# Kernel optimization log

Hardware: AMD Instinct MI355X
Metric: run time of the kernel (lower is better)

The kernel has to match this reference:

```python
import jax, jax.numpy as jnp
import numpy as np

B, T, R, A = 4, 40, 2000, 36864
H = W = 64
C = 256
PP = 7
RED = 16.0
NCLS = 21
NPOS = 64   # rois_per_image*B//4
NNEG = 192  # rois_per_image*B*3//4
DH = 1024

def _iou(b1, b2):
    # boxes are (top,left,bottom,right)
    t = jnp.maximum(b1[..., 0], b2[..., 0])
    l = jnp.maximum(b1[..., 1], b2[..., 1])
    b = jnp.minimum(b1[..., 2], b2[..., 2])
    r = jnp.minimum(b1[..., 3], b2[..., 3])
    inter = jnp.clip(b - t, 0.0) * jnp.clip(r - l, 0.0)
    a1 = (b1[..., 2] - b1[..., 0]) * (b1[..., 3] - b1[..., 1])
    a2 = (b2[..., 2] - b2[..., 0]) * (b2[..., 3] - b2[..., 1])
    return inter / (a1 + a2 - inter)

def _smooth_l1(p, t):
    d = jnp.abs(p - t)
    return jnp.mean(jnp.where(d < 1.0, 0.5 * d * d, d - 0.5))

def _roi_pool(fm, rois):
    # fm [B,C,H,W], rois [N,5] = (img_id, top,left,bottom,right) in feature-map coords
    fmt = jnp.transpose(fm, (0, 2, 3, 1))  # [B,H,W,C]
    n = rois[:, 0].astype(jnp.int32)[:, None, None]
    t, l, b, r = rois[:, 1], rois[:, 2], rois[:, 3], rois[:, 4]
    g = (jnp.arange(PP, dtype=fm.dtype) + 0.5) / PP
    ys = jnp.clip(t[:, None] + g * (b - t)[:, None], 0.0, H - 1.0)
    xs = jnp.clip(l[:, None] + g * (r - l)[:, None], 0.0, W - 1.0)
    y0 = jnp.floor(ys).astype(jnp.int32)
    x0 = jnp.floor(xs).astype(jnp.int32)
    y1 = jnp.minimum(y0 + 1, H - 1)
    x1 = jnp.minimum(x0 + 1, W - 1)
    wy = (ys - y0)[:, :, None, None]
    wx = (xs - x0)[:, None, :, None]
    def gat(yi, xi):
        return fmt[n, yi[:, :, None], xi[:, None, :], :]  # [N,PP,PP,C]
    v = (gat(y0, x0) * (1 - wy) * (1 - wx) + gat(y0, x1) * (1 - wy) * wx
         + gat(y1, x0) * wy * (1 - wx) + gat(y1, x1) * wy * wx)
    return v.reshape(v.shape[0], -1)  # [N, PP*PP*C]

def _forward(nms_reg, nms_cls, feature_maps, bboxes, classes, anchors, rpn_reg, rpn_cls, W1, b1, Wr, br, Wc, bc):
    # ---------------- RPN trainer: anchor/target matching ----------------
    iou_a = _iou(bboxes[:, :, None, :], anchors[None, None, :, :])   # [B,T,A]
    max_iou = jnp.max(iou_a, axis=1)                                  # [B,A]
    tidx = jnp.argmax(iou_a, axis=1)
    max_tgt = jnp.take_along_axis(bboxes, jnp.broadcast_to(tidx[:, :, None], (B, A, 4)), axis=1)
    mask = (max_iou > 0.5).reshape(-1)
    pos = jnp.nonzero(mask, size=128)[0]        # first 128 positives, flat order (matches cls[mask][:128])
    neg = jnp.nonzero(~mask, size=256 - B)[0]   # torch quirk: 256 - len(mask_matched) = 256 - B
    clsf = rpn_cls.reshape(-1)
    logits = jnp.concatenate([clsf[pos], clsf[neg]])
    lbl = jnp.concatenate([jnp.ones(128, dtype=logits.dtype), jnp.zeros(256 - B, dtype=logits.dtype)])
    rpn_cls_loss = jnp.mean(jnp.maximum(logits, 0) - logits * lbl + jnp.log1p(jnp.exp(-jnp.abs(logits))))
    anc_f = jnp.broadcast_to(anchors[None], (B, A, 4)).reshape(-1, 4)
    rpn_reg_loss = _smooth_l1(rpn_reg.reshape(-1, 4)[pos], max_tgt.reshape(-1, 4)[pos] - anc_f[pos]) / 4.0

    # ------------- RCNN trainer: proposal matching + sampling -------------
    iou_r = _iou(nms_reg[:, None, :, :], bboxes[:, :, None, :])  # [B,T,R]
    iou_m = jnp.max(iou_r, axis=1)                               # [B,R]
    ridx = jnp.argmax(iou_r, axis=1)
    iou_f = iou_m.reshape(-1)
    posr = jnp.nonzero(iou_f > 0.5, size=NPOS)[0]                # first NPOS positives, flat order
    negscore = jnp.where(iou_f <= 0.5, iou_f, -jnp.inf)
    negr = jax.lax.top_k(negscore, NNEG)[1]                      # negatives sorted by IoU descending
    cls_g = jnp.take_along_axis(classes, ridx, axis=1).reshape(-1)
    cls_s = jnp.concatenate([cls_g[posr], jnp.zeros(NNEG, dtype=cls_g.dtype)])
    imid = jnp.repeat(jnp.arange(B, dtype=nms_reg.dtype), R)
    nmsf = nms_reg.reshape(-1, 4)
    sel = jnp.concatenate([posr, negr])
    rois = jnp.concatenate([imid[sel][:, None], nmsf[sel]], axis=1)  # [256,5]
    feat = _roi_pool(feature_maps, rois)
    hmid = jax.nn.relu(feat @ W1 + b1)
    rreg = hmid @ Wr + br
    rcls = hmid @ Wc + bc
    logp = jax.nn.log_softmax(rcls, axis=-1)
    rcnn_cls_loss = -jnp.mean(jnp.take_along_axis(logp, cls_s[:, None], axis=1))
    posb = nmsf[posr]
    rounded = jnp.concatenate([jnp.floor(posb[:, :2] * RED), jnp.ceil(posb[:, 2:] * RED)], axis=1) / RED
    mb = jnp.take_along_axis(bboxes, jnp.broadcast_to(ridx[:, :, None], (B, R, 4)), axis=1).reshape(-1, 4)[posr]
    tgt = mb - rounded
    pr = rreg[:NPOS]
    rcnn_reg_loss = sum(_smooth_l1(pr[:, c], tgt[:, c]) for c in range(4)) / 4.0
    offset = sum(jnp.mean(jnp.abs(pr[:, c] - tgt[:, c])) for c in range(4)) / 4.0
    acc = jnp.mean((jnp.argmax(rcls[:NPOS], axis=-1) == cls_s[:NPOS]).astype(jnp.float32))
    return rpn_cls_loss, rpn_reg_loss, rcnn_cls_loss, rcnn_reg_loss, acc, offset

def _boxes(k, shape):
    k1, k2 = jax.random.split(k)
    c = jax.random.uniform(k1, shape + (2,), minval=10.0, maxval=54.0)
    h = jax.random.uniform(k2, shape + (2,), minval=3.0, maxval=8.0)
    return jnp.concatenate([c - h, c + h], axis=-1)  # (top,left,bottom,right)

def setup_inputs():
    key = jax.random.key(0)
    ks = jax.random.split(key, 13)
    base = _boxes(ks[0], (T,))
    shift = jax.random.uniform(ks[1], (B, T, 2), minval=-0.2, maxval=0.2)
    bboxes = base[None] + jnp.concatenate([shift, shift], axis=-1)  # guarantees >=128 RPN positives
    classes = jax.random.randint(ks[2], (B, T), 1, NCLS)
    anchors = _boxes(ks[3], (A,)).at[:T].set(base)
    nms_reg = _boxes(ks[4], (B, R))
    shift2 = jax.random.uniform(ks[5], (B, T, 2), minval=-0.1, maxval=0.1)
    nms_reg = nms_reg.at[:, :T].set(bboxes + jnp.concatenate([shift2, shift2], axis=-1))  # >=64 RCNN positives
    nms_cls = jax.random.normal(ks[6], (B, R))
    feature_maps = jax.random.normal(ks[7], (B, C, H, W))
    rpn_reg = 0.1 * jax.random.normal(ks[8], (B, A, 4))
    rpn_cls = jax.random.normal(ks[9], (B, A))
    D = PP * PP * C
    W1 = jax.random.normal(ks[10], (D, DH)) * float(1.0 / np.sqrt(D))
    b1 = jnp.zeros((DH,))
    Wr = jax.random.normal(ks[11], (DH, 4)) * float(1.0 / np.sqrt(DH))
    br = jnp.zeros((4,))
    Wc = jax.random.normal(ks[12], (DH, NCLS)) * float(1.0 / np.sqrt(DH))
    bc = jnp.zeros((NCLS,))
    return dict(nms_reg=nms_reg, nms_cls=nms_cls, feature_maps=feature_maps, bboxes=bboxes,
                classes=classes, anchors=anchors, rpn_reg=rpn_reg, rpn_cls=rpn_cls,
                W1=W1, b1=b1, Wr=Wr, br=br, Wc=Wc, bc=bc)

def reference(nms_reg, nms_cls, feature_maps, bboxes, classes, anchors, rpn_reg, rpn_cls, W1, b1, Wr, br, Wc, bc):
    return _forward(nms_reg, nms_cls, feature_maps, bboxes, classes, anchors, rpn_reg, rpn_cls, W1, b1, Wr, br, Wc, bc)
```

## Files before the change

### kernel.cpp

```cpp
#include <hip/hip_runtime.h>

typedef unsigned short u16;
typedef unsigned long long u64;

constexpr int cB = 4, cT = 40, cR = 2000, cA = 36864;
constexpr int cH = 64, cW = 64, cC = 256, cPP = 7;
constexpr int cNCLS = 21, cNPOS = 64, cNNEG = 192, cDH = 1024;
constexpr int cD = cPP * cPP * cC;
constexpr int cBA = cB * cA;
constexpr int cBR = cB * cR;
constexpr int NW64 = cBA / 64;
constexpr int SPLITS = 14;
constexpr int KCH = cD / SPLITS;
constexpr int BK = 64;
constexpr int NITER = KCH / BK;
constexpr unsigned POSKEY = 0x007FFFFFu;

constexpr size_t O_TIDX  = 0;
constexpr size_t O_MASKW = 589824;
constexpr size_t O_KEYS  = 608256;
constexpr size_t O_RIDXG = 640256;
constexpr size_t O_SEL   = 672256;
constexpr size_t O_CLS   = 673280;
constexpr size_t O_ROIS  = 674304;
constexpr size_t O_TGT   = 678400;
constexpr size_t O_FMT   = 1048576;
constexpr size_t O_FEAT  = O_FMT + 8388608;
constexpr size_t O_CPART = O_FEAT + 6422528;

__device__ __forceinline__ float b2f(u16 u) {
  return __uint_as_float(((unsigned)u) << 16);
}
__device__ __forceinline__ u16 f2b(float f) {
  unsigned x = __float_as_uint(f);
  unsigned r = x + 0x7FFFu + ((x >> 16) & 1u);
  return (u16)(r >> 16);
}
__device__ __forceinline__ unsigned f2key(float f) {
  unsigned b = __float_as_uint(f);
  return b ^ ((b & 0x80000000u) ? 0xFFFFFFFFu : 0x80000000u);
}

typedef __attribute__((ext_vector_type(8))) short short8;
typedef __attribute__((ext_vector_type(4))) float f32x4;

__global__ __launch_bounds__(256) void k_front(
    const float* __restrict__ bboxes, const float* __restrict__ anchors,
    const float* __restrict__ nms_reg, const float* __restrict__ fm,
    int* __restrict__ tidx, u64* __restrict__ maskw,
    unsigned* __restrict__ keys, int* __restrict__ ridxg,
    u16* __restrict__ fmt) {
  __shared__ float sfm[64 * 65];
  int bid = blockIdx.x;
  if (bid < 576) {
    float* sb = sfm;
    int b = bid / 144;
    if (threadIdx.x < cT * 4) sb[threadIdx.x] = bboxes[b * cT * 4 + threadIdx.x];
    __syncthreads();
    int i = bid * 256 + threadIdx.x;
    int a = i - b * cA;
    float4 av = ((const float4*)anchors)[a];
    float at = av.x, al = av.y, ab = av.z, ar = av.w;
    float area_a = (ab - at) * (ar - al);
    float best = -1.0f; int bi = 0;
    for (int t = 0; t < cT; ++t) {
      float bt = sb[t * 4], bl = sb[t * 4 + 1], bbv = sb[t * 4 + 2], brv = sb[t * 4 + 3];
      float ih = fmaxf(fminf(bbv, ab) - fmaxf(bt, at), 0.0f);
      float iw = fmaxf(fminf(brv, ar) - fmaxf(bl, al), 0.0f);
      float inter = ih * iw;
      float a1 = (bbv - bt) * (brv - bl);
      float iou = inter / (a1 + area_a - inter);
      if (iou > best) { best = iou; bi = t; }
    }
    tidx[i] = bi;
    u64 bal = __ballot(best > 0.5f);
    if ((threadIdx.x & 63) == 0) maskw[i >> 6] = bal;
  } else if (bid < 608) {
    float* sb = sfm;
    for (int j = threadIdx.x; j < cB * cT * 4; j += 256) sb[j] = bboxes[j];
    __syncthreads();
    int i = (bid - 576) * 256 + threadIdx.x;
    if (i >= cBR) return;
    int b = i / cR;
    float4 nv = ((const float4*)nms_reg)[i];
    float nt = nv.x, nl = nv.y, nb = nv.z, nr = nv.w;
    float area_n = (nb - nt) * (nr - nl);
    float best = -1.0f; int bi = 0;
    for (int t = 0; t < cT; ++t) {
      const float* bx = &sb[(b * cT + t) * 4];
      float ih = fmaxf(fminf(bx[2], nb) - fmaxf(bx[0], nt), 0.0f);
      float iw = fmaxf(fminf(bx[3], nr) - fmaxf(bx[1], nl), 0.0f);
      float inter = ih * iw;
      float a1 = (bx[2] - bx[0]) * (bx[3] - bx[1]);
      float iou = inter / (a1 + area_n - inter);
      if (iou > best) { best = iou; bi = t; }
    }
    keys[i] = (best <= 0.5f) ? f2key(best) : POSKEY;
    ridxg[i] = bi;
  } else {
    int f = bid - 608;
    int b = f >> 8;
    int c0 = ((f >> 6) & 3) * 64;
    int p0 = (f & 63) * 64;
    int t = threadIdx.x;
    int pL = (t & 15) * 4, cL = t >> 4;
    #pragma unroll
    for (int i = 0; i < 4; ++i) {
      int c = cL + i * 16;
      float4 v = *(const float4*)&fm[((size_t)b * cC + c0 + c) * (cH * cW) + p0 + pL];
      sfm[c * 65 + pL] = v.x; sfm[c * 65 + pL + 1] = v.y;
      sfm[c * 65 + pL + 2] = v.z; sfm[c * 65 + pL + 3] = v.w;
    }
    __syncthreads();
    int pW = t >> 2, cg = (t & 3) * 16;
    unsigned pk[8];
    #pragma unroll
    for (int j = 0; j < 8; ++j) {
      unsigned lo = f2b(sfm[(cg + 2 * j) * 65 + pW]);
      unsigned hi = f2b(sfm[(cg + 2 * j + 1) * 65 + pW]);
      pk[j] = lo | (hi << 16);
    }
    u16* dst = &fmt[((size_t)b * (cH * cW) + p0 + pW) * cC + c0 + cg];
    *(uint4*)dst = *(uint4*)&pk[0];
    *(uint4*)(dst + 8) = *(uint4*)&pk[4];
  }
}

__global__ __launch_bounds__(1024) void k_select(
    const u64* __restrict__ maskw, const int* __restrict__ tidx,
    const float* __restrict__ rpn_cls, const float* __restrict__ rpn_reg,
    const float* __restrict__ bboxes, const float* __restrict__ anchors,
    const unsigned* __restrict__ keysg, const int* __restrict__ ridxg,
    const float* __restrict__ nms_reg, const int* __restrict__ classes,
    int* __restrict__ sel, int* __restrict__ cls_s,
    float* __restrict__ rois, float* __restrict__ tgt,
    float* __restrict__ out) {
  __shared__ __align__(16) char smem[50688];
  __shared__ float s_scalF[2];
  __shared__ int s_scalI[3];
  int tid = threadIdx.x, lane = tid & 63, w = tid >> 6;
  u64 lmask = (1ULL << lane) - 1ULL;

  if (blockIdx.x == 0) {
    if (tid < 4) out[2 + tid] = 0.0f;
    u64* s_w   = (u64*)smem;
    int* s_pre = (int*)(smem + 18432);
    int* s_cw  = (int*)(smem + 19008);
    int* s_pos = (int*)(smem + 19584);
    int* s_neg = (int*)(smem + 20096);
    for (int k = tid; k < NW64; k += 1024) s_w[k] = maskw[k];
    if (tid < 128) s_pos[tid] = 0;
    if (tid < 252) s_neg[tid] = 0;
    if (tid == 0) { s_scalF[0] = 0.0f; s_scalF[1] = 0.0f; }
    __syncthreads();
    if (tid < 144) {
      int c = 0;
      #pragma unroll
      for (int k2 = 0; k2 < 16; ++k2) c += __popcll(s_w[tid * 16 + k2]);
      s_cw[tid] = c;
    }
    __syncthreads();
    if (tid == 0) {
      int run = 0;
      for (int ch = 0; ch < 144; ++ch) { s_pre[ch] = run; run += s_cw[ch]; }
    }
    __syncthreads();
    for (int ch = w; ch < 144; ch += 16) {
      int pbase = s_pre[ch];
      int nbase = ch * 1024 - pbase;
      if (pbase >= 128 && nbase >= 252) continue;
      int pc = 0;
      #pragma unroll
      for (int s2 = 0; s2 < 16; ++s2) {
        u64 word = s_w[ch * 16 + s2];
        bool m = (word >> lane) & 1ULL;
        int prefP = __popcll(word & lmask);
        int idx = ch * 1024 + s2 * 64 + lane;
        if (m) {
          int g = pbase + pc + prefP;
          if (g < 128) s_pos[g] = idx;
        } else {
          int g = nbase + (s2 * 64 + lane) - (pc + prefP);
          if (g < 252) s_neg[g] = idx;
        }
        pc += __popcll(word);
      }
    }
    __syncthreads();
    if (tid < 380) {
      int flat; float lbl;
      if (tid < 128) { flat = s_pos[tid]; lbl = 1.0f; }
      else           { flat = s_neg[tid - 128]; lbl = 0.0f; }
      float l = rpn_cls[flat];
      float term = fmaxf(l, 0.0f) - l * lbl + log1pf(expf(-fabsf(l)));
      atomicAdd(&s_scalF[0], term);
    }
    if (tid < 512) {
      int j = tid >> 2, c = tid & 3;
      int flat = s_pos[j];
      int b = flat / cA, a = flat - b * cA;
      int t = tidx[flat];
      float p = rpn_reg[flat * 4 + c];
      float tg = bboxes[(b * cT + t) * 4 + c] - anchors[a * 4 + c];
      float d = fabsf(p - tg);
      float sl = (d < 1.0f) ? 0.5f * d * d : d - 0.5f;
      atomicAdd(&s_scalF[1], sl);
    }
    __syncthreads();
    if (tid == 0) {
      out[0] = s_scalF[0] / 380.0f;
      out[1] = s_scalF[1] / 512.0f / 4.0f;
    }
  } else {
    unsigned* s_key = (unsigned*)smem;
    int* s_hist = (int*)(smem + 32000);
    int* s_pc   = (int*)(smem + 48384);
    int* s_wsum = (int*)(smem + 48896);
    int* s_wsuf = (int*)(smem + 48960);
    int* s_posr = (int*)(smem + 49024);
    int* s_negr = (int*)(smem + 49280);

    for (int i = tid; i < cBR; i += 1024) s_key[i] = keysg[i];
    if (tid < 64) s_posr[tid] = 0;
    __syncthreads();

    {
      int myv = 0; int mypre[8];
      #pragma unroll
      for (int p = 0; p < 8; ++p) {
        int i = p * 1024 + tid;
        bool v = (i < cBR) && (s_key[i] == POSKEY);
        u64 bal = __ballot(v);
        if (lane == 0) s_pc[p * 16 + w] = __popcll(bal);
        mypre[p] = __popcll(bal & lmask);
        myv |= v ? (1 << p) : 0;
      }
      __syncthreads();
      if (tid == 0) {
        int run = 0;
        for (int k = 0; k < 128; ++k) { int t = s_pc[k]; s_pc[k] = run; run += t; }
      }
      __syncthreads();
      #pragma unroll
      for (int p = 0; p < 8; ++p) {
        if (myv & (1 << p)) {
          int g = s_pc[p * 16 + w] + mypre[p];
          if (g < 64) s_posr[g] = p * 1024 + tid;
        }
      }
    }

    unsigned thr = 0; int G = 0;
    int need = cNNEG;
    #pragma unroll
    for (int lvl = 0; lvl < 3; ++lvl) {
      __syncthreads();
      #pragma unroll
      for (int k = 0; k < 4; ++k) s_hist[tid * 4 + k] = 0;
      __syncthreads();
      #pragma unroll
      for (int p = 0; p < 8; ++p) {
        int i = p * 1024 + tid;
        if (i < cBR) {
          unsigned key = s_key[i];
          int bkt = -1;
          if (lvl == 0) bkt = key >> 20;
          else if (lvl == 1) { if ((key >> 20) == (thr >> 20)) bkt = (key >> 8) & 0xFFF; }
          else { if ((key >> 8) == (thr >> 8)) bkt = (key & 0xFF) << 4; }
          if (bkt >= 0) atomicAdd(&s_hist[bkt], 1);
        }
      }
      __syncthreads();
      int local0 = s_hist[tid * 4 + 0], local1 = s_hist[tid * 4 + 1];
      int local2 = s_hist[tid * 4 + 2], local3 = s_hist[tid * 4 + 3];
      int lsum = local0 + local1 + local2 + local3;
      int x = lsum;
      #pragma unroll
      for (int off = 1; off < 64; off <<= 1) {
        int t = __shfl_down(x, off, 64);
        if (lane + off < 64) x += t;
      }
      if (lane == 0) s_wsum[w] = x;
      __syncthreads();
      if (tid == 0) {
        int run = 0;
        for (int wi = 15; wi >= 0; --wi) { s_wsuf[wi] = run; run += s_wsum[wi]; }
      }
      __syncthreads();
      int above = s_wsuf[w] + (x - lsum);
      int run = above;
      int loc[4] = {local3, local2, local1, local0};
      #pragma unroll
      for (int j = 0; j < 4; ++j) {
        int S = run + loc[j];
        if (run < need && S >= need) { s_scalI[0] = tid * 4 + (3 - j); s_scalI[1] = run; }
        run = S;
      }
      __syncthreads();
      int bS = s_scalI[0], ov = s_scalI[1];
      if (lvl == 0) thr = ((unsigned)bS) << 20;
      else if (lvl == 1) thr |= ((unsigned)bS) << 8;
      else thr |= ((unsigned)bS) >> 4;
      G += ov;
      need -= ov;
    }

    if (tid == 0) s_scalI[2] = 0;
    __syncthreads();
    #pragma unroll
    for (int p = 0; p < 8; ++p) {
      int i = p * 1024 + tid;
      if (i < cBR && s_key[i] > thr) {
        int slot = atomicAdd(&s_scalI[2], 1);
        s_negr[slot] = i;
      }
    }
    {
      __syncthreads();
      int myv = 0; int mypre[8];
      #pragma unroll
      for (int p = 0; p < 8; ++p) {
        int i = p * 1024 + tid;
        bool v = (i < cBR) && (s_key[i] == thr);
        u64 bal = __ballot(v);
        if (lane == 0) s_pc[p * 16 + w] = __popcll(bal);
        mypre[p] = __popcll(bal & lmask);
        myv |= v ? (1 << p) : 0;
      }
      __syncthreads();
      if (tid == 0) {
        int run = 0;
        for (int k = 0; k < 128; ++k) { int t = s_pc[k]; s_pc[k] = run; run += t; }
      }
      __syncthreads();
      #pragma unroll
      for (int p = 0; p < 8; ++p) {
        if (myv & (1 << p)) {
          int g = s_pc[p * 16 + w] + mypre[p];
          if (g < need) s_negr[G + g] = p * 1024 + tid;
        }
      }
    }
    __syncthreads();

    if (tid < 256) {
      int flat = (tid < 64) ? s_posr[tid] : s_negr[tid - 64];
      sel[tid] = flat;
      int b = flat / cR;
      #pragma unroll
      for (int c = 0; c < 4; ++c) rois[tid * 4 + c] = nms_reg[flat * 4 + c];
      cls_s[tid] = (tid < 64) ? classes[b * cT + ridxg[flat]] : 0;
      if (tid < 64) {
        int mt = ridxg[flat];
        #pragma unroll
        for (int c = 0; c < 4; ++c) {
          float v = nms_reg[flat * 4 + c];
          float rr = ((c < 2) ? floorf(v * 16.0f) : ceilf(v * 16.0f)) / 16.0f;
          float mbv = bboxes[(b * cT + mt) * 4 + c];
          tgt[tid * 4 + c] = mbv - rr;
        }
      }
    }
  }
}

__global__ void k_roi_pool(const u16* __restrict__ fmt, const float* __restrict__ rois,
                           const int* __restrict__ sel, u16* __restrict__ feat) {
  int j = blockIdx.x;
  int py = blockIdx.y;
  int c = threadIdx.x;
  int flat = sel[j];
  int n = flat / cR;
  float t = rois[j * 4 + 0], l = rois[j * 4 + 1];
  float bb = rois[j * 4 + 2], r = rois[j * 4 + 3];
  const u16* base = fmt + (size_t)n * (cH * cW) * cC;
  float gy = (py + 0.5f) / (float)cPP;
  float ys = fminf(fmaxf(t + gy * (bb - t), 0.0f), 63.0f);
  int y0 = (int)floorf(ys);
  int y1 = min(y0 + 1, 63);
  float wy = ys - (float)y0;
  #pragma unroll
  for (int px = 0; px < cPP; ++px) {
    float gx = (px + 0.5f) / (float)cPP;
    float xs = fminf(fmaxf(l + gx * (r - l), 0.0f), 63.0f);
    int x0 = (int)floorf(xs);
    int x1 = min(x0 + 1, 63);
    float wx = xs - (float)x0;
    float f00 = b2f(base[(y0 * cW + x0) * cC + c]);
    float f01 = b2f(base[(y0 * cW + x1) * cC + c]);
    float f10 = b2f(base[(y1 * cW + x0) * cC + c]);
    float f11 = b2f(base[(y1 * cW + x1) * cC + c]);
    float v = f00 * (1.0f - wy) * (1.0f - wx) + f01 * (1.0f - wy) * wx +
              f10 * wy * (1.0f - wx) + f11 * wy * wx;
    feat[((size_t)j * 49 + py * cPP + px) * cC + c] = f2b(v);
  }
}

__global__ __launch_bounds__(256) void k_gemm1(const u16* __restrict__ feat, const float* __restrict__ W1,
                                               float* __restrict__ Cpart) {
  __shared__ u16 Bs[2][32][64];
  int tid = threadIdx.x;
  int bid = blockIdx.x;
  int ksp = bid >> 5;
  int n0 = (bid & 31) * 32;
  int kb0 = ksp * KCH;
  int lane = tid & 63, w = tid >> 6;
  int r = lane & 15, q = lane >> 4;
  int rb = r & 7;

  f32x4 acc[4][2] = {};

  int bn = tid & 31, kq = tid >> 5;
  int bswz = (kq ^ (bn & 7)) * 8;
  const float* bp = &W1[(size_t)(kb0 + kq * 8) * cDH + n0 + bn];

  int offK0 = (q ^ rb) * 8;
  int offK1 = ((4 + q) ^ rb) * 8;

  const u16* afp = &feat[(size_t)(w * 64 + r) * cD + kb0 + q * 8];

  float fE[8], fO[8];
  short8 aE[4][2], aO[4][2];

#define LOADB(f) { \
    _Pragma("unroll") \
    for (int j = 0; j < 8; ++j) f[j] = bp[(size_t)j * cDH]; \
    bp += (size_t)BK * cDH; }
#define STOREB(buf, f) { \
    union { u16 u[8]; uint4 v; } pb; \
    _Pragma("unroll") \
    for (int j = 0; j < 8; ++j) pb.u[j] = f2b(f[j]); \
    *(uint4*)&Bs[buf][bn][bswz] = pb.v; }
#define LOADA(dst, itv) { \
    const u16* _p = afp + (itv) * 64; \
    _Pragma("unroll") \
    for (int mf = 0; mf < 4; ++mf) { \
      dst[mf][0] = *(const short8*)(_p + (size_t)mf * 16 * cD); \
      dst[mf][1] = *(const short8*)(_p + (size_t)mf * 16 * cD + 32); \
    } }
#define COMPUTE(buf, a) { \
    short8 b00 = *(const short8*)&Bs[buf][r][offK0]; \
    short8 b10 = *(const short8*)&Bs[buf][16 + r][offK0]; \
    short8 b01 = *(const short8*)&Bs[buf][r][offK1]; \
    short8 b11 = *(const short8*)&Bs[buf][16 + r][offK1]; \
    _Pragma("unroll") \
    for (int mf = 0; mf < 4; ++mf) { \
      acc[mf][0] = __builtin_amdgcn_mfma_f32_16x16x32_bf16(a[mf][0], b00, acc[mf][0], 0, 0, 0); \
      acc[mf][1] = __builtin_amdgcn_mfma_f32_16x16x32_bf16(a[mf][0], b10, acc[mf][1], 0, 0, 0); \
      acc[mf][0] = __builtin_amdgcn_mfma_f32_16x16x32_bf16(a[mf][1], b01, acc[mf][0], 0, 0, 0); \
      acc[mf][1] = __builtin_amdgcn_mfma_f32_16x16x32_bf16(a[mf][1], b11, acc[mf][1], 0, 0, 0); \
    } }

  LOADB(fE);
  LOADB(fO);
  STOREB(0, fE);
  LOADA(aE, 0);
  LOADB(fE);
  __syncthreads();

  for (int it = 0; it < NITER; it += 2) {
    STOREB(1, fO);
    if (it + 3 < NITER) LOADB(fO);
    LOADA(aO, it + 1);
    COMPUTE(0, aE);
    __syncthreads();
    if (it + 2 < NITER) {
      STOREB(0, fE);
      if (it + 4 < NITER) LOADB(fE);
      LOADA(aE, it + 2);
    }
    COMPUTE(1, aO);
    __syncthreads();
  }

#undef LOADB
#undef STOREB
#undef LOADA
#undef COMPUTE

  float* Cp = Cpart + (size_t)ksp * 256 * cDH;
  #pragma unroll
  for (int mf = 0; mf < 4; ++mf) {
    #pragma unroll
    for (int rg = 0; rg < 4; ++rg) {
      int row = w * 64 + mf * 16 + q * 4 + rg;
      Cp[(size_t)row * cDH + n0 + r] = acc[mf][0][rg];
      Cp[(size_t)row * cDH + n0 + 16 + r] = acc[mf][1][rg];
    }
  }
}

__global__ __launch_bounds__(256) void k_heads(
    const float* __restrict__ Cpart, const float* __restrict__ b1,
    const float* __restrict__ Wr, const float* __restrict__ br,
    const float* __restrict__ Wc, const float* __restrict__ bc,
    const int* __restrict__ cls_s, const float* __restrict__ tgt,
    float* __restrict__ out) {
  __shared__ float sacc[25];
  int row = blockIdx.x, tid = threadIdx.x, lane = tid & 63;
  if (tid < 25) sacc[tid] = 0.0f;
  __syncthreads();
  int k0 = tid * 4;
  float4 h = *(const float4*)&b1[k0];
  #pragma unroll
  for (int s = 0; s < SPLITS; ++s) {
    float4 c = *(const float4*)&Cpart[(size_t)s * 256 * cDH + (size_t)row * cDH + k0];
    h.x += c.x; h.y += c.y; h.z += c.z; h.w += c.w;
  }
  float hv[4] = {fmaxf(h.x, 0.f), fmaxf(h.y, 0.f), fmaxf(h.z, 0.f), fmaxf(h.w, 0.f)};
  float part[25];
  #pragma unroll
  for (int c = 0; c < 25; ++c) part[c] = 0.0f;
  #pragma unroll
  for (int j = 0; j < 4; ++j) {
    float4 wr = *(const float4*)&Wr[(k0 + j) * 4];
    part[0] += hv[j] * wr.x; part[1] += hv[j] * wr.y;
    part[2] += hv[j] * wr.z; part[3] += hv[j] * wr.w;
    const float* wc = &Wc[(k0 + j) * 21];
    #pragma unroll
    for (int c = 0; c < 21; ++c) part[4 + c] += hv[j] * wc[c];
  }
  #pragma unroll
  for (int off = 32; off; off >>= 1) {
    #pragma unroll
    for (int c = 0; c < 25; ++c) part[c] += __shfl_down(part[c], off, 64);
  }
  if (lane == 0) {
    #pragma unroll
    for (int c = 0; c < 25; ++c) atomicAdd(&sacc[c], part[c]);
  }
  __syncthreads();
  if (tid == 0) {
    int cls = cls_s[row];
    float m = -INFINITY;
    float vals[21];
    #pragma unroll
    for (int c = 0; c < 21; ++c) { vals[c] = sacc[4 + c] + bc[c]; m = fmaxf(m, vals[c]); }
    float sum = 0.0f;
    #pragma unroll
    for (int c = 0; c < 21; ++c) sum += expf(vals[c] - m);
    float lse = m + logf(sum);
    atomicAdd(&out[2], (lse - vals[cls]) * (1.0f / 256.0f));
    if (row < 64) {
      int am2 = 0; float bv = vals[0];
      #pragma unroll
      for (int c = 1; c < 21; ++c) if (vals[c] > bv) { bv = vals[c]; am2 = c; }
      if (am2 == cls) atomicAdd(&out[4], 1.0f / 64.0f);
    }
  }
  if (tid == 1 && row < 64) {
    float sl = 0.0f, of = 0.0f;
    #pragma unroll
    for (int c = 0; c < 4; ++c) {
      float d = fabsf((sacc[c] + br[c]) - tgt[row * 4 + c]);
      sl += (d < 1.0f) ? 0.5f * d * d : d - 0.5f;
      of += d;
    }
    atomicAdd(&out[3], sl * (1.0f / 256.0f));
    atomicAdd(&out[5], of * (1.0f / 256.0f));
  }
}

extern "C" void kernel_launch(void* const* d_in, const int* in_sizes, int n_in,
                              void* d_out, int out_size, void* d_ws, size_t ws_size,
                              hipStream_t stream) {
  const float* nms_reg = (const float*)d_in[0];
  const float* fm      = (const float*)d_in[2];
  const float* bboxes  = (const float*)d_in[3];
  const int*   classes = (const int*)d_in[4];
  const float* anchors = (const float*)d_in[5];
  const float* rpn_reg = (const float*)d_in[6];
  const float* rpn_cls = (const float*)d_in[7];
  const float* W1      = (const float*)d_in[8];
  const float* b1      = (const float*)d_in[9];
  const float* Wr      = (const float*)d_in[10];
  const float* br      = (const float*)d_in[11];
  const float* Wc      = (const float*)d_in[12];
  const float* bc      = (const float*)d_in[13];
  float* out = (float*)d_out;
  char* ws = (char*)d_ws;

  int*      tidx  = (int*)(ws + O_TIDX);
  u64*      maskw = (u64*)(ws + O_MASKW);
  unsigned* keys  = (unsigned*)(ws + O_KEYS);
  int*      ridxg = (int*)(ws + O_RIDXG);
  int*      sel   = (int*)(ws + O_SEL);
  int*      clss  = (int*)(ws + O_CLS);
  float*    rois  = (float*)(ws + O_ROIS);
  float*    tgt   = (float*)(ws + O_TGT);
  u16*      fmt   = (u16*)(ws + O_FMT);
  u16*      feat  = (u16*)(ws + O_FEAT);
  float*    Cpart = (float*)(ws + O_CPART);

  k_front<<<608 + 1024, 256, 0, stream>>>(bboxes, anchors, nms_reg, fm,
                                          tidx, maskw, keys, ridxg, fmt);
  k_select<<<2, 1024, 0, stream>>>(maskw, tidx, rpn_cls, rpn_reg, bboxes, anchors,
                                   keys, ridxg, nms_reg, classes, sel, clss, rois, tgt, out);
  k_roi_pool<<<dim3(256, cPP), 256, 0, stream>>>(fmt, rois, sel, feat);
  k_gemm1<<<448, 256, 0, stream>>>(feat, W1, Cpart);
  k_heads<<<256, 256, 0, stream>>>(Cpart, b1, Wr, br, Wc, bc, clss, tgt, out);
}
```

Before: 192.6 us.

## Deepen gemm1 prefetch pipeline with 4-stage B registers and manual barriers

Restructures the W1 x features GEMM main loop. B loads are now prefetched four stages ahead into a register ring, and A loads two stages ahead, in a fully unrolled loop. __syncthreads is replaced by an explicit lgkmcnt wait plus s_barrier and sched_barrier. MFMA sections run under raised s_setprio. The aim is to hide global-memory latency of the strided fp32 W1 reads, at the cost of more VGPR pressure and a larger unrolled code footprint.

```diff
diff --git a/kernel.cpp b/kernel.cpp
--- a/kernel.cpp
+++ b/kernel.cpp
@@ -412,71 +412,68 @@
 
   int bn = tid & 31, kq = tid >> 5;
   int bswz = (kq ^ (bn & 7)) * 8;
-  const float* bp = &W1[(size_t)(kb0 + kq * 8) * cDH + n0 + bn];
+  const float* bp0 = &W1[(size_t)(kb0 + kq * 8) * cDH + n0 + bn];
 
   int offK0 = (q ^ rb) * 8;
   int offK1 = ((4 + q) ^ rb) * 8;
 
   const u16* afp = &feat[(size_t)(w * 64 + r) * cD + kb0 + q * 8];
 
-  float fE[8], fO[8];
-  short8 aE[4][2], aO[4][2];
-
-#define LOADB(f) { \
+  float BR[4][8];
+  short8 A[2][4][2];
+
+#define LOADB(slot, ph) { const float* _bp = bp0 + (size_t)(ph) * BK * cDH; \
     _Pragma("unroll") \
-    for (int j = 0; j < 8; ++j) f[j] = bp[(size_t)j * cDH]; \
-    bp += (size_t)BK * cDH; }
-#define STOREB(buf, f) { \
+    for (int j = 0; j < 8; ++j) BR[slot][j] = _bp[(size_t)j * cDH]; }
+#define STOREB(buf, slot) { \
     union { u16 u[8]; uint4 v; } pb; \
     _Pragma("unroll") \
-    for (int j = 0; j < 8; ++j) pb.u[j] = f2b(f[j]); \
+    for (int j = 0; j < 8; ++j) pb.u[j] = f2b(BR[slot][j]); \
     *(uint4*)&Bs[buf][bn][bswz] = pb.v; }
-#define LOADA(dst, itv) { \
-    const u16* _p = afp + (itv) * 64; \
+#define LOADA(set, ph) { const u16* _p = afp + (ph) * 64; \
     _Pragma("unroll") \
     for (int mf = 0; mf < 4; ++mf) { \
-      dst[mf][0] = *(const short8*)(_p + (size_t)mf * 16 * cD); \
-      dst[mf][1] = *(const short8*)(_p + (size_t)mf * 16 * cD + 32); \
+      A[set][mf][0] = *(const short8*)(_p + (size_t)mf * 16 * cD); \
+      A[set][mf][1] = *(const short8*)(_p + (size_t)mf * 16 * cD + 32); \
     } }
-#define COMPUTE(buf, a) { \
+#define COMPUTE(buf, set) { \
     short8 b00 = *(const short8*)&Bs[buf][r][offK0]; \
     short8 b10 = *(const short8*)&Bs[buf][16 + r][offK0]; \
     short8 b01 = *(const short8*)&Bs[buf][r][offK1]; \
     short8 b11 = *(const short8*)&Bs[buf][16 + r][offK1]; \
     _Pragma("unroll") \
     for (int mf = 0; mf < 4; ++mf) { \
-      acc[mf][0] = __builtin_amdgcn_mfma_f32_16x16x32_bf16(a[mf][0], b00, acc[mf][0], 0, 0, 0); \
-      acc[mf][1] = __builtin_amdgcn_mfma_f32_16x16x32_bf16(a[mf][0], b10, acc[mf][1], 0, 0, 0); \
-      acc[mf][0] = __builtin_amdgcn_mfma_f32_16x16x32_bf16(a[mf][1], b01, acc[mf][0], 0, 0, 0); \
-      acc[mf][1] = __builtin_amdgcn_mfma_f32_16x16x32_bf16(a[mf][1], b11, acc[mf][1], 0, 0, 0); \
+      acc[mf][0] = __builtin_amdgcn_mfma_f32_16x16x32_bf16(A[set][mf][0], b00, acc[mf][0], 0, 0, 0); \
+      acc[mf][1] = __builtin_amdgcn_mfma_f32_16x16x32_bf16(A[set][mf][0], b10, acc[mf][1], 0, 0, 0); \
+      acc[mf][0] = __builtin_amdgcn_mfma_f32_16x16x32_bf16(A[set][mf][1], b01, acc[mf][0], 0, 0, 0); \
+      acc[mf][1] = __builtin_amdgcn_mfma_f32_16x16x32_bf16(A[set][mf][1], b11, acc[mf][1], 0, 0, 0); \
     } }
-
-  LOADB(fE);
-  LOADB(fO);
-  STOREB(0, fE);
-  LOADA(aE, 0);
-  LOADB(fE);
-  __syncthreads();
-
-  for (int it = 0; it < NITER; it += 2) {
-    STOREB(1, fO);
-    if (it + 3 < NITER) LOADB(fO);
-    LOADA(aO, it + 1);
-    COMPUTE(0, aE);
-    __syncthreads();
-    if (it + 2 < NITER) {
-      STOREB(0, fE);
-      if (it + 4 < NITER) LOADB(fE);
-      LOADA(aE, it + 2);
-    }
-    COMPUTE(1, aO);
-    __syncthreads();
+#define BARRIER() { \
+    asm volatile("s_waitcnt lgkmcnt(0)" ::: "memory"); \
+    __builtin_amdgcn_s_barrier(); \
+    __builtin_amdgcn_sched_barrier(0); }
+
+  LOADB(0, 0); LOADB(1, 1); LOADB(2, 2); LOADB(3, 3);
+  LOADA(0, 0); LOADA(1, 1);
+  STOREB(0, 0);
+  BARRIER();
+
+  #pragma unroll
+  for (int p = 0; p < NITER; ++p) {
+    if (p + 1 < NITER) STOREB((p + 1) & 1, (p + 1) & 3);
+    if (p + 4 < NITER) LOADB(p & 3, p + 4);
+    __builtin_amdgcn_s_setprio(1);
+    COMPUTE(p & 1, p & 1);
+    __builtin_amdgcn_s_setprio(0);
+    if (p + 2 < NITER) LOADA(p & 1, p + 2);
+    BARRIER();
   }
 
 #undef LOADB
 #undef STOREB
 #undef LOADA
 #undef COMPUTE
+#undef BARRIER
 
   float* Cp = Cpart + (size_t)ksp * 256 * cDH;
   #pragma unroll
```

Result: no change. 189.9 us (-1.4%).
